# Performance work log

Measured on AMD Instinct MI355X. Metric: run time of the kernel, lower is better.

Reference implementation:

```python
import jax, jax.numpy as jnp
import numpy as np

B, N, E, D = 32, 4096, 8192, 128


def setup_inputs() -> dict:
    key = jax.random.key(0)
    ks = jax.random.split(key, 6)
    atom_state = jax.random.normal(ks[0], (B, N, D), dtype=jnp.float32)
    messages = jax.random.normal(ks[1], (B, E, D), dtype=jnp.float32)
    connectivity = jax.random.randint(ks[2], (B, E, 2), 0, N, dtype=jnp.int32)
    kernel = jax.random.normal(ks[3], (D, 3 * D), dtype=jnp.float32) * 0.05
    recurrent_kernel = jax.random.normal(ks[4], (D, 3 * D), dtype=jnp.float32) * 0.05
    bias = jnp.zeros((2, 3 * D), dtype=jnp.float32)
    return {"atom_state": atom_state, "messages": messages,
            "connectivity": connectivity, "kernel": kernel,
            "recurrent_kernel": recurrent_kernel, "bias": bias}


def reference(atom_state, messages, connectivity, kernel, recurrent_kernel, bias):
    b, n, d = atom_state.shape
    # --- Reduce: scatter-add messages onto target atoms ---
    tgt_idx = connectivity[:, :, 1]                       # [B,E]
    offset = (jnp.arange(b, dtype=tgt_idx.dtype) * n)[:, None]
    flat_idx = (tgt_idx + offset).reshape(-1)             # [B*E]
    flat_msgs = messages.reshape(-1, d)                   # [B*E,D]
    aggregated = jax.ops.segment_sum(flat_msgs, flat_idx, num_segments=b * n)  # [B*N,D]
    # --- GRUCell (Keras default: reset_after=True, sigmoid/tanh) ---
    h = atom_state.reshape(-1, d)                         # [B*N,D]
    matrix_x = aggregated @ kernel + bias[0]              # [B*N,3D]
    matrix_h = h @ recurrent_kernel + bias[1]             # [B*N,3D]
    x_z, x_r, x_h = jnp.split(matrix_x, 3, axis=-1)
    r_z, r_r, r_h = jnp.split(matrix_h, 3, axis=-1)
    z = jax.nn.sigmoid(x_z + r_z)
    r = jax.nn.sigmoid(x_r + r_r)
    hh = jnp.tanh(x_h + r * r_h)
    h_new = z * h + (1.0 - z) * hh
    return h_new.reshape(b, n, d)
```

## Files before the change

### kernel.cpp

```cpp
#include <hip/hip_runtime.h>
#include <hip/hip_bf16.h>
#include <stdint.h>

#define BB 32
#define NN 4096
#define EE 8192
#define DD 128
#define MM (BB * NN)
#define THREE_D (3 * DD)
#define CAP 32

typedef __bf16 bf16x8 __attribute__((ext_vector_type(8)));
typedef __bf16 bf16x2 __attribute__((ext_vector_type(2)));
typedef float  f32x4  __attribute__((ext_vector_type(4)));
typedef float  f32x2  __attribute__((ext_vector_type(2)));

#define AGG_BYTES ((size_t)MM * DD * 2)
#define WT_OFF    AGG_BYTES
#define WT_BYTES  ((size_t)2 * THREE_D * DD * 2)
#define CNT_OFF   (WT_OFF + WT_BYTES)
#define CNT_BYTES ((size_t)MM * 4)
#define BKT_OFF   (CNT_OFF + CNT_BYTES)

__global__ void transpose_weights(const float* __restrict__ w0,
                                  const float* __restrict__ w1,
                                  __bf16* __restrict__ wt,
                                  int* __restrict__ counts) {
    int tid = blockIdx.x * blockDim.x + threadIdx.x;
    for (int i = tid; i < MM; i += 2 * THREE_D * DD)
        counts[i] = 0;
    int mat = tid / (THREE_D * DD);
    int rem = tid % (THREE_D * DD);
    int col = rem / DD;
    int k   = rem % DD;
    const float* src = mat ? w1 : w0;
    wt[tid] = (__bf16)src[k * THREE_D + col];
}

__global__ void scatter_ids(const int* __restrict__ conn,
                            int* __restrict__ counts,
                            int* __restrict__ bucket) {
    int e = blockIdx.x * 256 + threadIdx.x;
    int b = e >> 13;
    int2 pr = ((const int2*)conn)[e];
    int node = b * NN + pr.y;
    int pos = atomicAdd(&counts[node], 1);
    if (pos < CAP) bucket[node * CAP + pos] = e;
}

__global__ void gather_messages(const float* __restrict__ messages,
                                const int* __restrict__ counts,
                                const int* __restrict__ bucket,
                                __bf16* __restrict__ agg) {
    int node = __builtin_amdgcn_readfirstlane(blockIdx.x * 16 + (threadIdx.x >> 6));
    int lane = threadIdx.x & 63;
    int cnt = counts[node];
    if (cnt > CAP) cnt = CAP;
    const int* bp = bucket + (size_t)node * CAP;
    float a0 = 0.f, a1 = 0.f;
    int i = 0;
    for (; i + 2 <= cnt; i += 2) {
        int e0 = bp[i];
        int e1 = bp[i + 1];
        f32x2 v0 = *(const f32x2*)(messages + (size_t)e0 * DD + lane * 2);
        f32x2 v1 = *(const f32x2*)(messages + (size_t)e1 * DD + lane * 2);
        a0 += v0[0] + v1[0];
        a1 += v0[1] + v1[1];
    }
    if (i < cnt) {
        int e = bp[i];
        f32x2 v = *(const f32x2*)(messages + (size_t)e * DD + lane * 2);
        a0 += v[0];
        a1 += v[1];
    }
    bf16x2 o;
    o[0] = (__bf16)a0;
    o[1] = (__bf16)a1;
    *(bf16x2*)(agg + (size_t)node * DD + lane * 2) = o;
}

#define TPB_GEMM 8
__launch_bounds__(512, 2)
__global__ void gru_gemm_wreg(const __bf16* __restrict__ agg,
                              const float* __restrict__ h_in,
                              const __bf16* __restrict__ wt,
                              const float* __restrict__ bias,
                              float* __restrict__ out) {
    const int wave = threadIdx.x >> 6;
    const int lane = threadIdx.x & 63;
    const int quad = lane >> 4;
    const int l16  = lane & 15;

    bf16x8 bfrag[3][2][4];
    for (int p = 0; p < 3; ++p)
        for (int m = 0; m < 2; ++m)
            for (int ko = 0; ko < 4; ++ko)
                bfrag[p][m][ko] = *(const bf16x8*)(wt
                    + ((size_t)(m * THREE_D + p * 128 + wave * 16 + l16)) * DD
                    + ko * 32 + quad * 8);

    const int j = wave * 16 + l16;
    const float b0z = bias[j];
    const float b0r = bias[DD + j];
    const float b0h = bias[2 * DD + j];
    const float b1z = bias[THREE_D + j];
    const float b1r = bias[THREE_D + DD + j];
    const float b1h = bias[THREE_D + 2 * DD + j];

    const int tile0 = blockIdx.x * TPB_GEMM;

    bf16x8 a_raw[4];
    f32x4  h_raw[8];
    auto load_tile = [&](int tb) {
        int r = tb * 16 + l16;
        const __bf16* arow = agg  + (size_t)r * DD;
        const float*  hrow = h_in + (size_t)r * DD;
        for (int ko = 0; ko < 4; ++ko) {
            int k = ko * 32 + quad * 8;
            a_raw[ko]         = *(const bf16x8*)(arow + k);
            h_raw[ko * 2]     = *(const f32x4*)(hrow + k);
            h_raw[ko * 2 + 1] = *(const f32x4*)(hrow + k + 4);
        }
    };

    load_tile(tile0);
    for (int t = 0; t < TPB_GEMM; ++t) {
        const int tb = tile0 + t;

        f32x4 acc[3][2];
        for (int p = 0; p < 3; ++p)
            for (int m = 0; m < 2; ++m)
                acc[p][m] = (f32x4){0.f, 0.f, 0.f, 0.f};

        for (int ko = 0; ko < 4; ++ko) {
            bf16x8 hg;
            for (int i = 0; i < 4; ++i) {
                hg[i]     = (__bf16)h_raw[ko * 2][i];
                hg[i + 4] = (__bf16)h_raw[ko * 2 + 1][i];
            }
            for (int p = 0; p < 3; ++p) {
                acc[p][0] = __builtin_amdgcn_mfma_f32_16x16x32_bf16(
                    a_raw[ko], bfrag[p][0][ko], acc[p][0], 0, 0, 0);
                acc[p][1] = __builtin_amdgcn_mfma_f32_16x16x32_bf16(
                    hg,        bfrag[p][1][ko], acc[p][1], 0, 0, 0);
            }
        }

        if (t + 1 < TPB_GEMM) load_tile(tb + 1);

        for (int rr = 0; rr < 4; ++rr) {
            int row = tb * 16 + quad * 4 + rr;
            float xz  = acc[0][0][rr] + b0z;
            float rz  = acc[0][1][rr] + b1z;
            float xr  = acc[1][0][rr] + b0r;
            float rrg = acc[1][1][rr] + b1r;
            float xh  = acc[2][0][rr] + b0h;
            float rh  = acc[2][1][rr] + b1h;
            float z   = 1.f / (1.f + __expf(-(xz + rz)));
            float rg  = 1.f / (1.f + __expf(-(xr + rrg)));
            float pre = xh + rg * rh;
            float hh  = 2.f / (1.f + __expf(-2.f * pre)) - 1.f;
            float hold = h_in[(size_t)row * DD + j];
            float o = z * hold + (1.f - z) * hh;
            out[(size_t)row * DD + j] = o;
        }
    }
}

extern "C" void kernel_launch(void* const* d_in, const int* in_sizes, int n_in,
                              void* d_out, int out_size, void* d_ws, size_t ws_size,
                              hipStream_t stream) {
    const float* atom_state = (const float*)d_in[0];
    const float* messages   = (const float*)d_in[1];
    const int*   conn       = (const int*)d_in[2];
    const float* w0         = (const float*)d_in[3];
    const float* w1         = (const float*)d_in[4];
    const float* bias       = (const float*)d_in[5];
    float* out = (float*)d_out;

    __bf16* agg    = (__bf16*)d_ws;
    __bf16* wt     = (__bf16*)((char*)d_ws + WT_OFF);
    int*    counts = (int*)((char*)d_ws + CNT_OFF);
    int*    bucket = (int*)((char*)d_ws + BKT_OFF);

    transpose_weights<<<(2 * THREE_D * DD) / 256, 256, 0, stream>>>(w0, w1, wt, counts);
    scatter_ids<<<(BB * EE) / 256, 256, 0, stream>>>(conn, counts, bucket);
    gather_messages<<<MM / 16, 1024, 0, stream>>>(messages, counts, bucket, agg);
    gru_gemm_wreg<<<MM / (16 * TPB_GEMM), 512, 0, stream>>>(agg, atom_state, wt, bias, out);
}
```

Baseline: 391.0 us.

## Stage GEMM input tiles through double-buffered LDS shared across waves

In the old GRU GEMM kernel, all 8 waves each loaded the same 16-row agg and h tile from global memory. Now the block loads each tile once, cooperatively and coalesced, into a double-buffered shared-memory area, and each wave reads its MFMA fragments from LDS. The next tile's global load is issued before the current tile's compute to overlap latency. The old-h value in the epilogue is also read from LDS instead of global memory. This cuts redundant global and L2 traffic, at the cost of barriers, LDS usage and extra register staging.

```diff
diff --git a/kernel.cpp b/kernel.cpp
--- a/kernel.cpp
+++ b/kernel.cpp
@@ -80,16 +80,22 @@
 }
 
 #define TPB_GEMM 8
+#define AGP 136
+#define HP  132
 __launch_bounds__(512, 2)
-__global__ void gru_gemm_wreg(const __bf16* __restrict__ agg,
+__global__ void gru_gemm_pipe(const __bf16* __restrict__ agg,
                               const float* __restrict__ h_in,
                               const __bf16* __restrict__ wt,
                               const float* __restrict__ bias,
                               float* __restrict__ out) {
-    const int wave = threadIdx.x >> 6;
-    const int lane = threadIdx.x & 63;
+    const int tid  = threadIdx.x;
+    const int wave = tid >> 6;
+    const int lane = tid & 63;
     const int quad = lane >> 4;
     const int l16  = lane & 15;
+
+    __shared__ __bf16 aT[2][16 * AGP];
+    __shared__ float  hT[2][16 * HP];
 
     bf16x8 bfrag[3][2][4];
     for (int p = 0; p < 3; ++p)
@@ -109,23 +115,26 @@
 
     const int tile0 = blockIdx.x * TPB_GEMM;
 
-    bf16x8 a_raw[4];
-    f32x4  h_raw[8];
-    auto load_tile = [&](int tb) {
-        int r = tb * 16 + l16;
-        const __bf16* arow = agg  + (size_t)r * DD;
-        const float*  hrow = h_in + (size_t)r * DD;
-        for (int ko = 0; ko < 4; ++ko) {
-            int k = ko * 32 + quad * 8;
-            a_raw[ko]         = *(const bf16x8*)(arow + k);
-            h_raw[ko * 2]     = *(const f32x4*)(hrow + k);
-            h_raw[ko * 2 + 1] = *(const f32x4*)(hrow + k + 4);
-        }
+    bf16x8 sa;
+    f32x4  sh;
+    auto load_regs = [&](int tb) {
+        if (tid < 256)
+            sa = *(const bf16x8*)(agg + (size_t)tb * 2048 + tid * 8);
+        sh = *(const f32x4*)(h_in + (size_t)tb * 2048 + tid * 4);
     };
-
-    load_tile(tile0);
+    auto write_lds = [&](int buf) {
+        if (tid < 256)
+            *(bf16x8*)&aT[buf][(tid >> 4) * AGP + (tid & 15) * 8] = sa;
+        *(f32x4*)&hT[buf][(tid >> 5) * HP + (tid & 31) * 4] = sh;
+    };
+
+    load_regs(tile0);
+    write_lds(0);
+    int buf = 0;
     for (int t = 0; t < TPB_GEMM; ++t) {
+        __syncthreads();
         const int tb = tile0 + t;
+        if (t + 1 < TPB_GEMM) load_regs(tb + 1);
 
         f32x4 acc[3][2];
         for (int p = 0; p < 3; ++p)
@@ -133,23 +142,25 @@
                 acc[p][m] = (f32x4){0.f, 0.f, 0.f, 0.f};
 
         for (int ko = 0; ko < 4; ++ko) {
+            bf16x8 af = *(const bf16x8*)&aT[buf][l16 * AGP + ko * 32 + quad * 8];
+            f32x4 h0 = *(const f32x4*)&hT[buf][l16 * HP + ko * 32 + quad * 8];
+            f32x4 h1 = *(const f32x4*)&hT[buf][l16 * HP + ko * 32 + quad * 8 + 4];
             bf16x8 hg;
             for (int i = 0; i < 4; ++i) {
-                hg[i]     = (__bf16)h_raw[ko * 2][i];
-                hg[i + 4] = (__bf16)h_raw[ko * 2 + 1][i];
+                hg[i]     = (__bf16)h0[i];
+                hg[i + 4] = (__bf16)h1[i];
             }
             for (int p = 0; p < 3; ++p) {
                 acc[p][0] = __builtin_amdgcn_mfma_f32_16x16x32_bf16(
-                    a_raw[ko], bfrag[p][0][ko], acc[p][0], 0, 0, 0);
+                    af, bfrag[p][0][ko], acc[p][0], 0, 0, 0);
                 acc[p][1] = __builtin_amdgcn_mfma_f32_16x16x32_bf16(
-                    hg,        bfrag[p][1][ko], acc[p][1], 0, 0, 0);
+                    hg, bfrag[p][1][ko], acc[p][1], 0, 0, 0);
             }
         }
 
-        if (t + 1 < TPB_GEMM) load_tile(tb + 1);
-
         for (int rr = 0; rr < 4; ++rr) {
-            int row = tb * 16 + quad * 4 + rr;
+            int rl  = quad * 4 + rr;
+            int row = tb * 16 + rl;
             float xz  = acc[0][0][rr] + b0z;
             float rz  = acc[0][1][rr] + b1z;
             float xr  = acc[1][0][rr] + b0r;
@@ -160,10 +171,13 @@
             float rg  = 1.f / (1.f + __expf(-(xr + rrg)));
             float pre = xh + rg * rh;
             float hh  = 2.f / (1.f + __expf(-2.f * pre)) - 1.f;
-            float hold = h_in[(size_t)row * DD + j];
+            float hold = hT[buf][rl * HP + j];
             float o = z * hold + (1.f - z) * hh;
             out[(size_t)row * DD + j] = o;
         }
+
+        if (t + 1 < TPB_GEMM) write_lds(buf ^ 1);
+        buf ^= 1;
     }
 }
 
@@ -186,5 +200,5 @@
     transpose_weights<<<(2 * THREE_D * DD) / 256, 256, 0, stream>>>(w0, w1, wt, counts);
     scatter_ids<<<(BB * EE) / 256, 256, 0, stream>>>(conn, counts, bucket);
     gather_messages<<<MM / 16, 1024, 0, stream>>>(messages, counts, bucket, agg);
-    gru_gemm_wreg<<<MM / (16 * TPB_GEMM), 512, 0, stream>>>(agg, atom_state, wt, bias, out);
-}
+    gru_gemm_pipe<<<MM / (16 * TPB_GEMM), 512, 0, stream>>>(agg, atom_state, wt, bias, out);
+}
```

Result: faster. 362.4 us (-7.3%).
